# Optimization experiments

Hardware: AMD Instinct MI355X
Metric: run time of the kernel (lower is better)

The kernel has to match this reference:

```python
import jax, jax.numpy as jnp
import numpy as np

N_HEAD = 16

def setup_inputs() -> dict:
    key = jax.random.key(0)
    k1, k2, k3 = jax.random.split(key, 3)
    B, K, C = 2, 2048, 1024
    x = jax.random.normal(k1, (B, K, C), dtype=jnp.float32)
    W_qkv = jax.random.normal(k2, (C, 3 * C), dtype=jnp.float32) * (1.0 / np.sqrt(C))
    b_qkv = jnp.zeros((3 * C,), dtype=jnp.float32)
    W_proj = jax.random.normal(k3, (C, C), dtype=jnp.float32) * (1.0 / np.sqrt(C))
    b_proj = jnp.zeros((C,), dtype=jnp.float32)
    return {"x": x, "W_qkv": W_qkv, "b_qkv": b_qkv, "W_proj": W_proj, "b_proj": b_proj, "K": K}

def reference(x, W_qkv, b_qkv, W_proj, b_proj, K):
    B, _, C = x.shape
    H = N_HEAD
    Dh = C // H
    qkv = x @ W_qkv + b_qkv                      # [B, K, 3C]
    q, k, v = jnp.split(qkv, 3, axis=-1)
    # [B, H, K, Dh]
    q = q.reshape(B, K, H, Dh).transpose(0, 2, 1, 3)
    k = k.reshape(B, K, H, Dh).transpose(0, 2, 1, 3)
    v = v.reshape(B, K, H, Dh).transpose(0, 2, 1, 3)
    att = jnp.einsum('bhqd,bhkd->bhqk', q, k) / jnp.sqrt(jnp.asarray(Dh, dtype=x.dtype))
    causal = jnp.tril(jnp.ones((K, K), dtype=bool))
    att = jnp.where(causal[None, None], att, jnp.asarray(-jnp.inf, dtype=x.dtype))
    att = jax.nn.softmax(att, axis=-1)
    y = jnp.einsum('bhqk,bhkd->bhqd', att, v)    # [B, H, K, Dh]
    y = y.transpose(0, 2, 1, 3).reshape(B, K, C)
    return y @ W_proj + b_proj
```

## Files before the change

kernel.cpp:

```cpp
#include <hip/hip_runtime.h>
#include <hip/hip_bf16.h>
#include <math.h>

typedef __attribute__((ext_vector_type(8))) short short8;
typedef __attribute__((ext_vector_type(4))) float f32x4;
typedef __attribute__((ext_vector_type(4))) short short4v;
typedef __attribute__((ext_vector_type(2))) int int2v;

static __device__ __forceinline__ short f2bf(float f) {
    __hip_bfloat16 h = __float2bfloat16(f);
    return *reinterpret_cast<short*>(&h);
}
static __device__ __forceinline__ void store_out(float* p, float v) { *p = v; }
static __device__ __forceinline__ void store_out(short* p, float v) { *p = f2bf(v); }

#define GLL16(g, l) __builtin_amdgcn_global_load_lds( \
    (const __attribute__((address_space(1))) void*)(g), \
    (__attribute__((address_space(3))) void*)(l), 16, 0, 0)

#if __has_builtin(__builtin_amdgcn_exp2f)
#define EXP2(x) __builtin_amdgcn_exp2f(x)
#else
#define EXP2(x) exp2f(x)
#endif

#if __has_builtin(__builtin_amdgcn_cvt_pk_bf16_f32)
typedef __attribute__((ext_vector_type(2))) __bf16 bf16x2;
static __device__ __forceinline__ int pack2bf(float a, float b) {
    bf16x2 r = __builtin_amdgcn_cvt_pk_bf16_f32(a, b);
    return __builtin_bit_cast(int, r);
}
#else
static __device__ __forceinline__ int pack2bf(float a, float b) {
    unsigned ua = __builtin_bit_cast(unsigned, a) + 0x8000u;
    unsigned ub = __builtin_bit_cast(unsigned, b) + 0x8000u;
    return (int)((ua >> 16) | (ub & 0xFFFF0000u));
}
#endif

static __device__ __forceinline__ void transpose_cast_tile(
    const float* __restrict__ W, short* __restrict__ Wt, int Kd, int N,
    int bx, int by)
{
    __shared__ float ts[32][33];
    const int c0 = bx * 32, r0 = by * 32;
    const int tx = threadIdx.x & 31, ty = threadIdx.x >> 5;
    #pragma unroll
    for (int e = 0; e < 4; ++e)
        ts[ty + e * 8][tx] = W[(size_t)(r0 + ty + e * 8) * N + c0 + tx];
    __syncthreads();
    #pragma unroll
    for (int e = 0; e < 4; ++e)
        Wt[(size_t)(c0 + ty + e * 8) * Kd + r0 + tx] = f2bf(ts[tx][ty + e * 8]);
}

__global__ __launch_bounds__(256) void prep_kernel(
    const float* __restrict__ x,      short* __restrict__ xb,    int nx,
    const float* __restrict__ W_qkv,  short* __restrict__ Wt1,
    const float* __restrict__ W_proj, short* __restrict__ Wt2,
    int C)
{
    const int nbx = nx / 1024;
    const int nb1 = (3 * C / 32) * (C / 32);
    int bid = blockIdx.x;
    if (bid < nbx) {
        int i = (bid * 256 + threadIdx.x) * 4;
        float4 v = *(const float4*)(x + i);
        short4v o = { f2bf(v.x), f2bf(v.y), f2bf(v.z), f2bf(v.w) };
        *(short4v*)(xb + i) = o;
        return;
    }
    bid -= nbx;
    if (bid < nb1) {
        const int nc = 3 * C / 32;
        transpose_cast_tile(W_qkv, Wt1, C, 3 * C, bid % nc, bid / nc);
        return;
    }
    bid -= nb1;
    {
        const int nc = C / 32;
        transpose_cast_tile(W_proj, Wt2, C, C, bid % nc, bid / nc);
    }
}

__global__ __launch_bounds__(256) void vtrans_kernel(
    const short* __restrict__ qkvb, short* __restrict__ vt, int K, int C)
{
    __shared__ short Vs[64][72];
    const int k0 = blockIdx.x * 64, h = blockIdx.y, b = blockIdx.z;
    const size_t rs = (size_t)3 * C;
    const short* src = qkvb + (size_t)b * K * rs + 2 * C + h * 64;
    const int key = threadIdx.x >> 3, d0 = (threadIdx.x & 7) * 8;
    *(short8*)&Vs[key][d0]      = *(const short8*)(src + (size_t)(k0 + key) * rs + d0);
    *(short8*)&Vs[key + 32][d0] = *(const short8*)(src + (size_t)(k0 + key + 32) * rs + d0);
    __syncthreads();
    const int d = threadIdx.x >> 2, kc = threadIdx.x & 3;
    short* dst = vt + ((size_t)(b * 16 + h) * 64 + d) * K + k0 + kc * 16;
    short8 o0, o1;
    #pragma unroll
    for (int j = 0; j < 8; ++j) { o0[j] = Vs[kc * 16 + j][d]; o1[j] = Vs[kc * 16 + 8 + j][d]; }
    *(short8*)dst = o0;
    *(short8*)(dst + 8) = o1;
}

#define GM 128
#define GN 128
#define GK 32

template <typename OutT>
__global__ __launch_bounds__(256) void gemm_mfma_kernel(
    const short* __restrict__ A, const short* __restrict__ Bt,
    const float* __restrict__ bias, OutT* __restrict__ C,
    int M, int N, int Kd, int qcols, float qscale)
{
    __shared__ __attribute__((aligned(16))) short As[GM * GK];
    __shared__ __attribute__((aligned(16))) short Bs[GN * GK];
    const int tid  = threadIdx.x;
    const int lane = tid & 63, w = tid >> 6;
    const int col  = lane & 15, quad = lane >> 4;
    const int wm = (w & 1) * 64, wn = (w >> 1) * 64;
    const int row0 = blockIdx.y * GM, col0 = blockIdx.x * GN;
    const float sc = (col0 < qcols) ? qscale : 1.f;

    const int sr = tid >> 2, scg = (tid & 3) * 8;
    const short* gA = A  + (size_t)(row0 + sr) * Kd + scg;
    const short* gB = Bt + (size_t)(col0 + sr) * Kd + scg;
    short* lA = As + sr * GK + scg;
    short* lB = Bs + sr * GK + scg;
    const size_t skip = (size_t)64 * Kd;

    f32x4 acc[4][4] = {};
    for (int k0 = 0; k0 < Kd; k0 += GK) {
        __syncthreads();
        GLL16(gA,        lA);
        GLL16(gA + skip, lA + 64 * GK);
        GLL16(gB,        lB);
        GLL16(gB + skip, lB + 64 * GK);
        gA += GK; gB += GK;
        __syncthreads();

        short8 aF[4], bF[4];
        #pragma unroll
        for (int mt = 0; mt < 4; ++mt)
            aF[mt] = *(const short8*)&As[(wm + mt * 16 + col) * GK + quad * 8];
        #pragma unroll
        for (int nt = 0; nt < 4; ++nt)
            bF[nt] = *(const short8*)&Bs[(wn + nt * 16 + col) * GK + quad * 8];
        #pragma unroll
        for (int mt = 0; mt < 4; ++mt)
            #pragma unroll
            for (int nt = 0; nt < 4; ++nt)
                acc[mt][nt] = __builtin_amdgcn_mfma_f32_16x16x32_bf16(aF[mt], bF[nt], acc[mt][nt], 0, 0, 0);
    }

    #pragma unroll
    for (int mt = 0; mt < 4; ++mt)
        #pragma unroll
        for (int i = 0; i < 4; ++i) {
            const size_t r = row0 + wm + mt * 16 + quad * 4 + i;
            #pragma unroll
            for (int nt = 0; nt < 4; ++nt) {
                const int c = col0 + wn + nt * 16 + col;
                store_out(&C[r * N + c], (acc[mt][nt][i] + bias[c]) * sc);
            }
        }
}

#define DH 64

__global__ __launch_bounds__(256, 2) void flash_mfma_kernel(
    const short* __restrict__ qkvb,
    const short* __restrict__ vt,
    short* __restrict__ y,
    int K, int C)
{
    __shared__ __attribute__((aligned(16))) short smem[37888];

    const int tid  = threadIdx.x;
    const int lane = tid & 63, w = tid >> 6;
    const int col  = lane & 15, quad = lane >> 4;

    short* Ksw = smem + w * 4160;
    short* Vsw = smem + 16640 + w * 4160;
    short* Ptw = smem + 33280 + w * 1152;
    float* Or  = (float*)smem;

    const int cmb = blockIdx.x & 31;
    const int g   = blockIdx.x >> 5;
    const int b   = cmb >> 4, h = cmb & 15;

    short8 bOnes;
    #pragma unroll
    for (int j = 0; j < 8; ++j) bOnes[j] = (col == 0) ? (short)0x3F80 : (short)0;

    const size_t rs = (size_t)3 * C;
    const short* qbase = qkvb + (size_t)b * K * rs + h * DH;
    const short* kbase = qbase + C;
    const short* vbase = vt + (size_t)(b * 16 + h) * DH * K;

    const int srow = lane & 56;
    const int goff = (lane & 7) * 8;
    const int loff = lane * 8;

    auto run = [&](int T) {
        const int t0 = T * 64;

        short8 aQ[4][2];
        #pragma unroll
        for (int qg = 0; qg < 4; ++qg) {
            const short* qp = qbase + (size_t)(t0 + qg * 16 + col) * rs;
            aQ[qg][0] = *(const short8*)(qp + quad * 8);
            aQ[qg][1] = *(const short8*)(qp + 32 + quad * 8);
        }
        f32x4 O[4][4] = {};
        f32x4 L4[4] = {};

        for (int ci = w; ci <= T; ci += 4) {
            const int kc = ci * 64;
            #pragma unroll
            for (int c2 = 0; c2 < 8; ++c2) {
                GLL16(kbase + (size_t)(kc + srow + c2) * rs + goff, Ksw + c2 * 520 + loff);
                GLL16(vbase + (size_t)(srow + c2) * K + kc + goff,  Vsw + c2 * 520 + loff);
            }
            asm volatile("s_waitcnt vmcnt(0)" ::: "memory");

            short8 bK[4][2], bV[4][2];
            #pragma unroll
            for (int nb = 0; nb < 4; ++nb) {
                const int ka = (4 * (col & 1) + nb) * 520 + (col >> 1) * 64 + quad * 8;
                bK[nb][0] = *(const short8*)&Ksw[ka];
                bK[nb][1] = *(const short8*)&Ksw[ka + 32];
            }
            #pragma unroll
            for (int db = 0; db < 4; ++db) {
                const int va = (col & 7) * 520 + (db * 2 + (col >> 3)) * 64 + quad * 8;
                bV[db][0] = *(const short8*)&Vsw[va];
                bV[db][1] = *(const short8*)&Vsw[va + 32];
            }

            const bool diag = (kc == t0);
            #pragma unroll
            for (int qg = 0; qg < 4; ++qg) {
                f32x4 S[4] = {};
                #pragma unroll
                for (int nb = 0; nb < 4; ++nb) {
                    S[nb] = __builtin_amdgcn_mfma_f32_16x16x32_bf16(aQ[qg][0], bK[nb][0], S[nb], 0, 0, 0);
                    S[nb] = __builtin_amdgcn_mfma_f32_16x16x32_bf16(aQ[qg][1], bK[nb][1], S[nb], 0, 0, 0);
                }
                if (!diag) {
                    #pragma unroll
                    for (int i = 0; i < 4; ++i) {
                        int2v pw = { pack2bf(EXP2(S[0][i]), EXP2(S[1][i])),
                                     pack2bf(EXP2(S[2][i]), EXP2(S[3][i])) };
                        *(int2v*)&Ptw[(quad * 4 + i) * 72 + col * 4] = pw;
                    }
                } else {
                    const int qrel = qg * 16 + quad * 4;
                    #pragma unroll
                    for (int i = 0; i < 4; ++i) {
                        float s0 = (col * 4 + 0 <= qrel + i) ? S[0][i] : -INFINITY;
                        float s1 = (col * 4 + 1 <= qrel + i) ? S[1][i] : -INFINITY;
                        float s2 = (col * 4 + 2 <= qrel + i) ? S[2][i] : -INFINITY;
                        float s3 = (col * 4 + 3 <= qrel + i) ? S[3][i] : -INFINITY;
                        int2v pw = { pack2bf(EXP2(s0), EXP2(s1)),
                                     pack2bf(EXP2(s2), EXP2(s3)) };
                        *(int2v*)&Ptw[(quad * 4 + i) * 72 + col * 4] = pw;
                    }
                }
                asm volatile("s_waitcnt lgkmcnt(0)" ::: "memory");
                #pragma unroll
                for (int half = 0; half < 2; ++half) {
                    short8 aP = *(const short8*)&Ptw[col * 72 + half * 32 + quad * 8];
                    #pragma unroll
                    for (int db = 0; db < 4; ++db)
                        O[qg][db] = __builtin_amdgcn_mfma_f32_16x16x32_bf16(aP, bV[db][half], O[qg][db], 0, 0, 0);
                    L4[qg] = __builtin_amdgcn_mfma_f32_16x16x32_bf16(aP, bOnes, L4[qg], 0, 0, 0);
                }
            }
        }

        __syncthreads();
        for (int ww = 0; ww < 4; ++ww) {
            if (w == ww) {
                #pragma unroll
                for (int qg = 0; qg < 4; ++qg)
                    #pragma unroll
                    for (int i = 0; i < 4; ++i) {
                        const int row = qg * 16 + quad * 4 + i;
                        #pragma unroll
                        for (int db = 0; db < 4; ++db) {
                            float v = O[qg][db][i];
                            if (ww == 0) Or[row * 68 + db * 16 + col] = v;
                            else         Or[row * 68 + db * 16 + col] += v;
                        }
                        if (col == 0) {
                            if (ww == 0) Or[row * 68 + 64] = L4[qg][i];
                            else         Or[row * 68 + 64] += L4[qg][i];
                        }
                    }
            }
            __syncthreads();
        }

        #pragma unroll
        for (int rstep = 0; rstep < 4; ++rstep) {
            const int row = w * 16 + rstep * 4 + quad;
            f32x4 ov = *(const f32x4*)&Or[row * 68 + col * 4];
            const float inv = 1.f / Or[row * 68 + 64];
            int2v o2 = { pack2bf(ov[0] * inv, ov[1] * inv),
                         pack2bf(ov[2] * inv, ov[3] * inv) };
            *(int2v*)(y + ((size_t)b * K + t0 + row) * C + h * DH + col * 4) = o2;
        }
        __syncthreads();
    };

    run(g);
    run(31 - g);
}

extern "C" void kernel_launch(void* const* d_in, const int* in_sizes, int n_in,
                              void* d_out, int out_size, void* d_ws, size_t ws_size,
                              hipStream_t stream)
{
    const float* x      = (const float*)d_in[0];
    const float* W_qkv  = (const float*)d_in[1];
    const float* b_qkv  = (const float*)d_in[2];
    const float* W_proj = (const float*)d_in[3];
    const float* b_proj = (const float*)d_in[4];

    const int B = 2, K = 2048, C = 1024, H = 16;
    const int M = B * K;
    const float C2 = 0.18033688f;

    char* ws = (char*)d_ws;
    short* xb    = (short*)ws;  ws += (size_t)M * C * 2;
    short* Wt1   = (short*)ws;  ws += (size_t)3 * C * C * 2;
    short* Wt2   = (short*)ws;  ws += (size_t)C * C * 2;
    short* qkvb  = (short*)ws;  ws += (size_t)M * 3 * C * 2;
    short* yb    = (short*)ws;  ws += (size_t)M * C * 2;
    short* vtb   = (short*)ws;

    const int nbx = (M * C) / 1024;
    const int nb1 = (3 * C / 32) * (C / 32);
    const int nb2 = (C / 32) * (C / 32);
    prep_kernel<<<nbx + nb1 + nb2, 256, 0, stream>>>(x, xb, M * C, W_qkv, Wt1, W_proj, Wt2, C);

    dim3 g1((3 * C) / GN, M / GM);
    gemm_mfma_kernel<short><<<g1, 256, 0, stream>>>(xb, Wt1, b_qkv, qkvb, M, 3 * C, C, C, C2);

    dim3 gv(K / 64, H, B);
    vtrans_kernel<<<gv, 256, 0, stream>>>(qkvb, vtb, K, C);

    const int NPAIR = (K / 64) / 2;
    flash_mfma_kernel<<<dim3(NPAIR * 32), 256, 0, stream>>>(qkvb, vtb, yb, K, C);

    dim3 g3(C / GN, M / GM);
    gemm_mfma_kernel<float><<<g3, 256, 0, stream>>>(yb, Wt2, b_proj, (float*)d_out, M, C, C, 0, 1.f);
}
```

Measured before the change: 192.9 us.

## Double-buffer per-wave K/V chunks with 32-key tiles in flash attention

Each wave now handles 32-key chunks instead of 64-key chunks and double-buffers its K/V staging in LDS. The next chunk's global-to-LDS loads are issued before the current one is computed, and only the older loads are waited on. This hides global load latency behind MFMA work and gives finer load balance across the four waves on the causal diagonal. In exchange it adds more loop iterations, per-chunk mask checks and extra LDS buffer indexing.

```diff
diff --git a/kernel.cpp b/kernel.cpp
--- a/kernel.cpp
+++ b/kernel.cpp
@@ -174,16 +174,15 @@
     short* __restrict__ y,
     int K, int C)
 {
-    __shared__ __attribute__((aligned(16))) short smem[37888];
+    __shared__ __attribute__((aligned(16))) short smem[35840];
 
     const int tid  = threadIdx.x;
     const int lane = tid & 63, w = tid >> 6;
     const int col  = lane & 15, quad = lane >> 4;
 
-    short* Ksw = smem + w * 4160;
-    short* Vsw = smem + 16640 + w * 4160;
-    short* Ptw = smem + 33280 + w * 1152;
-    float* Or  = (float*)smem;
+    short* Wreg = smem + w * 8320;
+    short* Ptw  = smem + 33280 + w * 640;
+    float* Or   = (float*)smem;
 
     const int cmb = blockIdx.x & 31;
     const int g   = blockIdx.x >> 5;
@@ -198,12 +197,25 @@
     const short* kbase = qbase + C;
     const short* vbase = vt + (size_t)(b * 16 + h) * DH * K;
 
-    const int srow = lane & 56;
-    const int goff = (lane & 7) * 8;
+    const int krow = (lane >> 3) * 4, koff = (lane & 7) * 8;
+    const int vrow = lane >> 2,       voff = (lane & 3) * 8;
     const int loff = lane * 8;
+
+    auto stage = [&](int ci, int buf) {
+        const int kc = ci * 32;
+        short* Kb = Wreg + buf * 4160;
+        short* Vb = Kb + 2080;
+        #pragma unroll
+        for (int c2 = 0; c2 < 4; ++c2)
+            GLL16(kbase + (size_t)(kc + krow + c2) * rs + koff, Kb + c2 * 520 + loff);
+        #pragma unroll
+        for (int c2 = 0; c2 < 4; ++c2)
+            GLL16(vbase + (size_t)(c2 * 16 + vrow) * K + kc + voff, Vb + c2 * 520 + loff);
+    };
 
     auto run = [&](int T) {
         const int t0 = T * 64;
+        const int NC = 2 * T + 2;
 
         short8 aQ[4][2];
         #pragma unroll
@@ -215,68 +227,65 @@
         f32x4 O[4][4] = {};
         f32x4 L4[4] = {};
 
-        for (int ci = w; ci <= T; ci += 4) {
-            const int kc = ci * 64;
-            #pragma unroll
-            for (int c2 = 0; c2 < 8; ++c2) {
-                GLL16(kbase + (size_t)(kc + srow + c2) * rs + goff, Ksw + c2 * 520 + loff);
-                GLL16(vbase + (size_t)(srow + c2) * K + kc + goff,  Vsw + c2 * 520 + loff);
-            }
-            asm volatile("s_waitcnt vmcnt(0)" ::: "memory");
-
-            short8 bK[4][2], bV[4][2];
-            #pragma unroll
-            for (int nb = 0; nb < 4; ++nb) {
-                const int ka = (4 * (col & 1) + nb) * 520 + (col >> 1) * 64 + quad * 8;
-                bK[nb][0] = *(const short8*)&Ksw[ka];
-                bK[nb][1] = *(const short8*)&Ksw[ka + 32];
-            }
-            #pragma unroll
-            for (int db = 0; db < 4; ++db) {
-                const int va = (col & 7) * 520 + (db * 2 + (col >> 3)) * 64 + quad * 8;
-                bV[db][0] = *(const short8*)&Vsw[va];
-                bV[db][1] = *(const short8*)&Vsw[va + 32];
-            }
-
-            const bool diag = (kc == t0);
+        int ci = w, buf = 0;
+        if (ci < NC) stage(ci, 0);
+        for (; ci < NC; ci += 4) {
+            const int kc = ci * 32;
+            const int nci = ci + 4;
+            if (nci < NC) {
+                stage(nci, buf ^ 1);
+                asm volatile("s_waitcnt vmcnt(8)" ::: "memory");
+            } else {
+                asm volatile("s_waitcnt vmcnt(0)" ::: "memory");
+            }
+            const short* Kb = Wreg + buf * 4160;
+            const short* Vb = Kb + 2080;
+
+            short8 bK[2][2], bV[4];
+            #pragma unroll
+            for (int nb = 0; nb < 2; ++nb) {
+                const int kl = col * 2 + nb;
+                const int ka = (kl & 3) * 520 + (kl >> 2) * 64 + quad * 8;
+                bK[nb][0] = *(const short8*)&Kb[ka];
+                bK[nb][1] = *(const short8*)&Kb[ka + 32];
+            }
+            #pragma unroll
+            for (int db = 0; db < 4; ++db)
+                bV[db] = *(const short8*)&Vb[db * 520 + col * 32 + quad * 8];
+
             #pragma unroll
             for (int qg = 0; qg < 4; ++qg) {
-                f32x4 S[4] = {};
+                const int qb = t0 + qg * 16;
+                f32x4 S[2] = {};
                 #pragma unroll
-                for (int nb = 0; nb < 4; ++nb) {
+                for (int nb = 0; nb < 2; ++nb) {
                     S[nb] = __builtin_amdgcn_mfma_f32_16x16x32_bf16(aQ[qg][0], bK[nb][0], S[nb], 0, 0, 0);
                     S[nb] = __builtin_amdgcn_mfma_f32_16x16x32_bf16(aQ[qg][1], bK[nb][1], S[nb], 0, 0, 0);
                 }
-                if (!diag) {
+                if (kc + 31 <= qb) {
+                    #pragma unroll
+                    for (int i = 0; i < 4; ++i)
+                        *(int*)&Ptw[(quad * 4 + i) * 40 + col * 2] =
+                            pack2bf(EXP2(S[0][i]), EXP2(S[1][i]));
+                } else {
+                    const int kg = kc + col * 2;
                     #pragma unroll
                     for (int i = 0; i < 4; ++i) {
-                        int2v pw = { pack2bf(EXP2(S[0][i]), EXP2(S[1][i])),
-                                     pack2bf(EXP2(S[2][i]), EXP2(S[3][i])) };
-                        *(int2v*)&Ptw[(quad * 4 + i) * 72 + col * 4] = pw;
-                    }
-                } else {
-                    const int qrel = qg * 16 + quad * 4;
-                    #pragma unroll
-                    for (int i = 0; i < 4; ++i) {
-                        float s0 = (col * 4 + 0 <= qrel + i) ? S[0][i] : -INFINITY;
-                        float s1 = (col * 4 + 1 <= qrel + i) ? S[1][i] : -INFINITY;
-                        float s2 = (col * 4 + 2 <= qrel + i) ? S[2][i] : -INFINITY;
-                        float s3 = (col * 4 + 3 <= qrel + i) ? S[3][i] : -INFINITY;
-                        int2v pw = { pack2bf(EXP2(s0), EXP2(s1)),
-                                     pack2bf(EXP2(s2), EXP2(s3)) };
-                        *(int2v*)&Ptw[(quad * 4 + i) * 72 + col * 4] = pw;
+                        const int q = qb + quad * 4 + i;
+                        float s0 = (kg + 0 <= q) ? S[0][i] : -INFINITY;
+                        float s1 = (kg + 1 <= q) ? S[1][i] : -INFINITY;
+                        *(int*)&Ptw[(quad * 4 + i) * 40 + col * 2] =
+                            pack2bf(EXP2(s0), EXP2(s1));
                     }
                 }
                 asm volatile("s_waitcnt lgkmcnt(0)" ::: "memory");
+                short8 aP = *(const short8*)&Ptw[col * 40 + quad * 8];
                 #pragma unroll
-                for (int half = 0; half < 2; ++half) {
-                    short8 aP = *(const short8*)&Ptw[col * 72 + half * 32 + quad * 8];
-                    #pragma unroll
-                    for (int db = 0; db < 4; ++db)
-                        O[qg][db] = __builtin_amdgcn_mfma_f32_16x16x32_bf16(aP, bV[db][half], O[qg][db], 0, 0, 0);
-                    L4[qg] = __builtin_amdgcn_mfma_f32_16x16x32_bf16(aP, bOnes, L4[qg], 0, 0, 0);
-                }
-            }
+                for (int db = 0; db < 4; ++db)
+                    O[qg][db] = __builtin_amdgcn_mfma_f32_16x16x32_bf16(aP, bV[db], O[qg][db], 0, 0, 0);
+                L4[qg] = __builtin_amdgcn_mfma_f32_16x16x32_bf16(aP, bOnes, L4[qg], 0, 0, 0);
+            }
+            buf ^= 1;
         }
 
         __syncthreads();
```

Measured after the change: 197.0 us. 1.02x slower.
